# Kernel tuning notes

Measured on AMD Instinct MI355X. Metric: run time of the kernel, lower is better.

The kernel has to match this reference:

```python
import jax, jax.numpy as jnp
import numpy as np

B, T, E, H = 4, 2048, 1024, 16
S = E // H  # 64


def setup_inputs() -> dict:
    key = jax.random.key(0)
    ks = jax.random.split(key, 6)
    return {
        "x": jax.random.normal(ks[0], (B, T, E), dtype=jnp.float32),
        "Wk": jax.random.normal(ks[1], (S, S), dtype=jnp.float32) * (1.0 / np.sqrt(S)),
        "Wq": jax.random.normal(ks[2], (S, S), dtype=jnp.float32) * (1.0 / np.sqrt(S)),
        "Wv": jax.random.normal(ks[3], (S, S), dtype=jnp.float32) * (1.0 / np.sqrt(S)),
        "Wp": jax.random.normal(ks[4], (E, E), dtype=jnp.float32) * (1.0 / np.sqrt(E)),
        "bp": jnp.zeros((E,), dtype=jnp.float32),
    }


def reference(x, Wk, Wq, Wv, Wp, bp):
    b, t, e = x.shape
    h, s = H, S
    xh = x.reshape(b, t, h, s)
    # per-head projections share one (s,s) weight across all heads (torch Linear: y = x @ W.T)
    keys = jnp.einsum('bthi,oi->bhto', xh, Wk)     # (b,h,t,s)
    queries = jnp.einsum('bthi,oi->bhto', xh, Wq)
    values = jnp.einsum('bthi,oi->bhto', xh, Wv)
    scale = e ** 0.25  # q and k each divided by e^(1/4) -> net 1/sqrt(e)
    queries = queries / scale
    keys = keys / scale
    dot = jnp.einsum('bhqs,bhks->bhqk', queries, keys)  # (b,h,t,t)
    attn = jax.nn.softmax(dot, axis=-1)
    out = jnp.einsum('bhqk,bhks->bqhs', attn, values)   # (b,t,h,s)
    out = out.reshape(b, t, h * s)
    return jnp.einsum('bte,oe->bto', out, Wp) + bp
```

## Files before the change

kernel.cpp:

```cpp
#include <hip/hip_runtime.h>

#define Bv 4
#define Tv 2048
#define Ev 1024
#define Hv 16
#define Sv 64

typedef __attribute__((ext_vector_type(8))) short bf16x8;
typedef __attribute__((ext_vector_type(4))) float f32x4;

__device__ __forceinline__ ushort f2bf(float f) {
    unsigned u = __float_as_uint(f);
    u = (u + 0x7FFFu + ((u >> 16) & 1u)) >> 16;
    return (ushort)u;
}
__device__ __forceinline__ unsigned pk2(float a, float b) {
    return (unsigned)f2bf(a) | ((unsigned)f2bf(b) << 16);
}
__device__ __forceinline__ unsigned pk2r(float a, float b) {
    return ((__float_as_uint(a) + 0x8000u) >> 16)
         | ((__float_as_uint(b) + 0x8000u) & 0xffff0000u);
}

__device__ __forceinline__ void async16(void* lds, const void* g) {
    __builtin_amdgcn_global_load_lds(
        (const __attribute__((address_space(1))) unsigned int*)g,
        (__attribute__((address_space(3))) unsigned int*)lds, 16, 0, 0);
}

__global__ __launch_bounds__(256) void cast_kernel(
    const float* __restrict__ Wp, const float* __restrict__ Wq,
    const float* __restrict__ Wk, const float* __restrict__ Wv,
    ushort* __restrict__ Wpb, ushort* __restrict__ Wqb,
    ushort* __restrict__ Wkb, ushort* __restrict__ Wvb)
{
    int blk = blockIdx.x;
    if (blk < 1024) {
        int i = (blk * 256 + threadIdx.x) * 4;
        float4 v = *(const float4*)(Wp + i);
        ushort4 o;
        o.x = f2bf(v.x); o.y = f2bf(v.y); o.z = f2bf(v.z); o.w = f2bf(v.w);
        *(ushort4*)(Wpb + i) = o;
    } else {
        int p = blk - 1024;
        const float* src = (p == 0) ? Wq : ((p == 1) ? Wk : Wv);
        ushort* dst      = (p == 0) ? Wqb : ((p == 1) ? Wkb : Wvb);
        const float scale = (p == 0) ? 0.03125f * 1.4426950408889634f : 1.0f;
        #pragma unroll
        for (int it = 0; it < 4; ++it) {
            int i = (it * 256 + threadIdx.x) * 4;
            float4 v = *(const float4*)(src + i);
            ushort4 o;
            o.x = f2bf(v.x * scale); o.y = f2bf(v.y * scale);
            o.z = f2bf(v.z * scale); o.w = f2bf(v.w * scale);
            *(ushort4*)(dst + i) = o;
        }
    }
}

__global__ __launch_bounds__(192) void qkv_kernel(
    const float* __restrict__ x,
    const ushort* __restrict__ Wqb, const ushort* __restrict__ Wkb,
    const ushort* __restrict__ Wvb,
    ushort* __restrict__ Q, ushort* __restrict__ K, ushort* __restrict__ Vt)
{
    const int tid  = threadIdx.x;
    const int wave = tid >> 6;
    const int lane = tid & 63;
    const int m    = lane & 15;
    const int quad = lane >> 4;

    const ushort* Wsel = (wave == 0) ? Wqb : ((wave == 1) ? Wkb : Wvb);
    bf16x8 wf[4][2];
    #pragma unroll
    for (int ot = 0; ot < 4; ++ot)
        #pragma unroll
        for (int ks = 0; ks < 2; ++ks)
            wf[ot][ks] = *(const bf16x8*)&Wsel[(ot * 16 + m) * 64 + ks * 32 + quad * 8];

    const int tt = blockIdx.x >> 2;
    const int hg = blockIdx.x & 3;
    const int g0 = tt * 16;
    const int gm = g0 + m;
    const int b  = g0 >> 11;
    const int t0 = g0 & 2047;

    #pragma unroll
    for (int hi = 0; hi < 4; ++hi) {
        const int h  = hg * 4 + hi;
        const int bh = b * Hv + h;

        bf16x8 xf[2];
        #pragma unroll
        for (int ks = 0; ks < 2; ++ks) {
            const float* src = x + (size_t)gm * Ev + h * Sv + ks * 32 + quad * 8;
            float4 v0 = *(const float4*)src;
            float4 v1 = *(const float4*)(src + 4);
            unsigned pk[4];
            pk[0] = pk2(v0.x, v0.y); pk[1] = pk2(v0.z, v0.w);
            pk[2] = pk2(v1.x, v1.y); pk[3] = pk2(v1.z, v1.w);
            xf[ks] = *(bf16x8*)pk;
        }

        f32x4 acc[4];
        #pragma unroll
        for (int ot = 0; ot < 4; ++ot) acc[ot] = (f32x4){0.f, 0.f, 0.f, 0.f};

        if (wave < 2) {
            #pragma unroll
            for (int ks = 0; ks < 2; ++ks)
                #pragma unroll
                for (int ot = 0; ot < 4; ++ot)
                    acc[ot] = __builtin_amdgcn_mfma_f32_16x16x32_bf16(
                        wf[ot][ks], xf[ks], acc[ot], 0, 0, 0);
            ushort* dst = ((wave == 0) ? Q : K)
                        + ((size_t)bh * Tv + t0 + m) * Sv + quad * 4;
            #pragma unroll
            for (int ot = 0; ot < 4; ++ot) {
                uint2 w;
                w.x = pk2(acc[ot][0], acc[ot][1]);
                w.y = pk2(acc[ot][2], acc[ot][3]);
                *(uint2*)(dst + ot * 16) = w;
            }
        } else {
            #pragma unroll
            for (int ks = 0; ks < 2; ++ks)
                #pragma unroll
                for (int st = 0; st < 4; ++st)
                    acc[st] = __builtin_amdgcn_mfma_f32_16x16x32_bf16(
                        xf[ks], wf[st][ks], acc[st], 0, 0, 0);
            ushort* vr = Vt + ((size_t)bh * Sv + m) * Tv + t0 + quad * 4;
            #pragma unroll
            for (int st = 0; st < 4; ++st) {
                uint2 w;
                w.x = pk2(acc[st][0], acc[st][1]);
                w.y = pk2(acc[st][2], acc[st][3]);
                *(uint2*)(vr + (size_t)st * 16 * Tv) = w;
            }
        }
    }
}

__global__ __launch_bounds__(256, 4) void attn_kernel(
    const ushort* __restrict__ Q, const ushort* __restrict__ K,
    const ushort* __restrict__ Vt, ushort* __restrict__ O)
{
    __shared__ ushort kl[64 * 64];
    __shared__ ushort vl[64 * 64];
    __shared__ ushort pl[4][32 * 64];

    const int tid  = threadIdx.x;
    const int wave = tid >> 6;
    const int lane = tid & 63;
    const int m    = lane & 15;
    const int quad = lane >> 4;
    const int bh   = blockIdx.x & 63;
    const int q0   = (blockIdx.x >> 6) << 7;

    const ushort* Qb = Q + ((size_t)bh * Tv + q0 + wave * 32) * Sv;
    bf16x8 qf[2][2];
    #pragma unroll
    for (int g = 0; g < 2; ++g)
        #pragma unroll
        for (int ks = 0; ks < 2; ++ks)
            qf[g][ks] = *(const bf16x8*)&Qb[(g * 16 + m) * Sv + ks * 32 + quad * 8];

    f32x4 oa[2][4];
    float lsum[2] = {0.f, 0.f};
    #pragma unroll
    for (int g = 0; g < 2; ++g)
        #pragma unroll
        for (int nt = 0; nt < 4; ++nt)
            oa[g][nt] = (f32x4){0.f, 0.f, 0.f, 0.f};

    const ushort* Kb = K  + (size_t)bh * Tv * Sv;
    const ushort* Vb = Vt + (size_t)bh * Sv * Tv;
    ushort* pw = pl[wave];

    const int r0 = tid >> 3,         cg0 = (tid & 7) ^ (r0 & 7);
    const int r1 = (256 + tid) >> 3, cg1 = ((256 + tid) & 7) ^ (r1 & 7);
    const size_t koff0 = (size_t)r0 * Sv + cg0 * 8;
    const size_t koff1 = (size_t)r1 * Sv + cg1 * 8;
    const size_t voff0 = (size_t)r0 * Tv + cg0 * 8;
    const size_t voff1 = (size_t)r1 * Tv + cg1 * 8;
    const int mx = m & 7;

    for (int k0 = 0; k0 < Tv; k0 += 64) {
        __syncthreads();
        async16(&kl[(size_t)tid * 8],         Kb + (size_t)k0 * Sv + koff0);
        async16(&kl[((size_t)tid + 256) * 8], Kb + (size_t)k0 * Sv + koff1);
        async16(&vl[(size_t)tid * 8],         Vb + k0 + voff0);
        async16(&vl[((size_t)tid + 256) * 8], Vb + k0 + voff1);
        __syncthreads();

        #pragma unroll
        for (int nt = 0; nt < 4; ++nt) {
            const int krow = nt * 16 + m;
            bf16x8 a0 = *(const bf16x8*)&kl[krow * 64 + ((quad       ^ mx) * 8)];
            bf16x8 a1 = *(const bf16x8*)&kl[krow * 64 + (((4 + quad) ^ mx) * 8)];
            #pragma unroll
            for (int g = 0; g < 2; ++g) {
                f32x4 s = (f32x4){0.f, 0.f, 0.f, 0.f};
                s = __builtin_amdgcn_mfma_f32_16x16x32_bf16(a0, qf[g][0], s, 0, 0, 0);
                s = __builtin_amdgcn_mfma_f32_16x16x32_bf16(a1, qf[g][1], s, 0, 0, 0);
                float p0 = __builtin_amdgcn_exp2f(s[0]);
                float p1 = __builtin_amdgcn_exp2f(s[1]);
                float p2 = __builtin_amdgcn_exp2f(s[2]);
                float p3 = __builtin_amdgcn_exp2f(s[3]);
                lsum[g] += (p0 + p1) + (p2 + p3);
                uint2 w;
                w.x = pk2r(p0, p1);
                w.y = pk2r(p2, p3);
                *(uint2*)&pw[(g * 16 + m) * 64
                             + (((nt * 2 + (quad >> 1)) ^ mx) * 8)
                             + (quad & 1) * 4] = w;
            }
        }

        bf16x8 af[2][2];
        #pragma unroll
        for (int g = 0; g < 2; ++g) {
            af[g][0] = *(const bf16x8*)&pw[(g * 16 + m) * 64 + ((quad       ^ mx) * 8)];
            af[g][1] = *(const bf16x8*)&pw[(g * 16 + m) * 64 + (((4 + quad) ^ mx) * 8)];
        }
        #pragma unroll
        for (int nt = 0; nt < 4; ++nt) {
            const int vrow = nt * 16 + m;
            bf16x8 v0 = *(const bf16x8*)&vl[vrow * 64 + ((quad       ^ mx) * 8)];
            bf16x8 v1 = *(const bf16x8*)&vl[vrow * 64 + (((4 + quad) ^ mx) * 8)];
            #pragma unroll
            for (int g = 0; g < 2; ++g) {
                oa[g][nt] = __builtin_amdgcn_mfma_f32_16x16x32_bf16(af[g][0], v0, oa[g][nt], 0, 0, 0);
                oa[g][nt] = __builtin_amdgcn_mfma_f32_16x16x32_bf16(af[g][1], v1, oa[g][nt], 0, 0, 0);
            }
        }
    }

    #pragma unroll
    for (int g = 0; g < 2; ++g) {
        lsum[g] += __shfl_xor(lsum[g], 16, 64);
        lsum[g] += __shfl_xor(lsum[g], 32, 64);
    }
    float* ll = (float*)pw;
    if (lane < 16) {
        ll[lane]      = 1.0f / lsum[0];
        ll[16 + lane] = 1.0f / lsum[1];
    }

    const int b = bh >> 4, h = bh & 15;
    #pragma unroll
    for (int g = 0; g < 2; ++g)
        #pragma unroll
        for (int nt = 0; nt < 4; ++nt)
            #pragma unroll
            for (int r = 0; r < 4; ++r)
                O[((size_t)(b * Tv + q0 + wave * 32 + g * 16 + quad * 4 + r)) * Ev
                  + h * Sv + nt * 16 + m]
                    = f2bf(oa[g][nt][r] * ll[g * 16 + quad * 4 + r]);
}

__global__ __launch_bounds__(256) void proj_kernel(
    const ushort* __restrict__ A, const ushort* __restrict__ B,
    const float* __restrict__ bp, float* __restrict__ C)
{
    __shared__ ushort Asm[128 * 32];
    __shared__ ushort Bsm[128 * 32];
    const int tid  = threadIdx.x;
    const int wave = tid >> 6;
    const int lane = tid & 63;
    const int m    = lane & 15;
    const int quad = lane >> 4;
    const int wm   = wave >> 1;
    const int wn   = wave & 1;
    const int m0   = blockIdx.x * 128;
    const int n0   = blockIdx.y * 128;

    f32x4 acc[4][4];
    #pragma unroll
    for (int i = 0; i < 4; ++i)
        #pragma unroll
        for (int j = 0; j < 4; ++j)
            acc[i][j] = (f32x4){0.f, 0.f, 0.f, 0.f};

    for (int k0 = 0; k0 < Ev; k0 += 32) {
        __syncthreads();
        #pragma unroll
        for (int j = 0; j < 2; ++j) {
            int c   = j * 256 + tid;
            int row = c >> 2;
            int col = (c & 3) * 8;
            async16(&Asm[c * 8], &A[(size_t)(m0 + row) * Ev + k0 + col]);
            async16(&Bsm[c * 8], &B[(size_t)(n0 + row) * Ev + k0 + col]);
        }
        __syncthreads();

        bf16x8 af[4], bf[4];
        #pragma unroll
        for (int i = 0; i < 4; ++i)
            af[i] = *(const bf16x8*)&Asm[(wm * 64 + i * 16 + m) * 32 + quad * 8];
        #pragma unroll
        for (int j = 0; j < 4; ++j)
            bf[j] = *(const bf16x8*)&Bsm[(wn * 64 + j * 16 + m) * 32 + quad * 8];
        #pragma unroll
        for (int i = 0; i < 4; ++i)
            #pragma unroll
            for (int j = 0; j < 4; ++j)
                acc[i][j] = __builtin_amdgcn_mfma_f32_16x16x32_bf16(
                    af[i], bf[j], acc[i][j], 0, 0, 0);
    }

    float bbv[4];
    #pragma unroll
    for (int j = 0; j < 4; ++j)
        bbv[j] = bp[n0 + wn * 64 + j * 16 + m];

    #pragma unroll
    for (int i = 0; i < 4; ++i)
        #pragma unroll
        for (int j = 0; j < 4; ++j)
            #pragma unroll
            for (int r = 0; r < 4; ++r)
                C[(size_t)(m0 + wm * 64 + i * 16 + quad * 4 + r) * Ev
                  + n0 + wn * 64 + j * 16 + m] = acc[i][j][r] + bbv[j];
}

extern "C" void kernel_launch(void* const* d_in, const int* in_sizes, int n_in,
                              void* d_out, int out_size, void* d_ws, size_t ws_size,
                              hipStream_t stream) {
    const float* x  = (const float*)d_in[0];
    const float* Wk = (const float*)d_in[1];
    const float* Wq = (const float*)d_in[2];
    const float* Wv = (const float*)d_in[3];
    const float* Wp = (const float*)d_in[4];
    const float* bp = (const float*)d_in[5];
    float* out = (float*)d_out;

    ushort* Q   = (ushort*)d_ws;
    ushort* K   = Q   + 8388608;
    ushort* Vt  = K   + 8388608;
    ushort* O   = Vt  + 8388608;
    ushort* Wpb = O   + 8388608;
    ushort* Wqb = Wpb + 1048576;
    ushort* Wkb = Wqb + 4096;
    ushort* Wvb = Wkb + 4096;

    cast_kernel<<<1027, 256, 0, stream>>>(Wp, Wq, Wk, Wv, Wpb, Wqb, Wkb, Wvb);
    qkv_kernel<<<2048, 192, 0, stream>>>(x, Wqb, Wkb, Wvb, Q, K, Vt);
    attn_kernel<<<1024, 256, 0, stream>>>(Q, K, Vt, O);
    proj_kernel<<<dim3(64, 8), 256, 0, stream>>>(O, Wpb, bp, out);
}
```

Baseline: 229.6 us.

## Keep softmax probabilities in registers and feed PV with 16x16x16 MFMA

The attention kernel no longer writes exponentiated scores to a per-wave LDS buffer and reads them back as MFMA operands. The S-accumulator layout is reused directly as the A operand of 16x16x16 bf16 MFMAs, with V fragments read from LDS in a matching layout. The bf16 packing helpers are replaced by a truncating perm for P and the library round-to-nearest conversion elsewhere. The change removes an LDS round trip and frees LDS, but uses twice as many smaller MFMA instructions and truncates P instead of rounding it.

```diff
diff --git a/kernel.cpp b/kernel.cpp
--- a/kernel.cpp
+++ b/kernel.cpp
@@ -1,4 +1,5 @@
 #include <hip/hip_runtime.h>
+#include <hip/hip_bf16.h>
 
 #define Bv 4
 #define Tv 2048
@@ -7,19 +8,33 @@
 #define Sv 64
 
 typedef __attribute__((ext_vector_type(8))) short bf16x8;
+typedef __attribute__((ext_vector_type(4))) short bf16x4;
 typedef __attribute__((ext_vector_type(4))) float f32x4;
+
+#if __has_builtin(__builtin_amdgcn_mfma_f32_16x16x16_bf16)
+#define MFMA161616(a, b, c) __builtin_amdgcn_mfma_f32_16x16x16_bf16(a, b, c, 0, 0, 0)
+#elif __has_builtin(__builtin_amdgcn_mfma_f32_16x16x16bf16_1k)
+#define MFMA161616(a, b, c) __builtin_amdgcn_mfma_f32_16x16x16bf16_1k(a, b, c, 0, 0, 0)
+#else
+__device__ __forceinline__ f32x4 mfma161616_asm(bf16x4 a, bf16x4 b, f32x4 c) {
+    f32x4 d;
+    asm("v_mfma_f32_16x16x16_bf16 %0, %1, %2, %3" : "=v"(d) : "v"(a), "v"(b), "v"(c));
+    return d;
+}
+#define MFMA161616(a, b, c) mfma161616_asm(a, b, c)
+#endif
 
 __device__ __forceinline__ ushort f2bf(float f) {
     unsigned u = __float_as_uint(f);
     u = (u + 0x7FFFu + ((u >> 16) & 1u)) >> 16;
     return (ushort)u;
 }
-__device__ __forceinline__ unsigned pk2(float a, float b) {
-    return (unsigned)f2bf(a) | ((unsigned)f2bf(b) << 16);
-}
-__device__ __forceinline__ unsigned pk2r(float a, float b) {
-    return ((__float_as_uint(a) + 0x8000u) >> 16)
-         | ((__float_as_uint(b) + 0x8000u) & 0xffff0000u);
+__device__ __forceinline__ unsigned pkrn(float a, float b) {
+    __hip_bfloat162 t = __float22bfloat162_rn(make_float2(a, b));
+    unsigned r; __builtin_memcpy(&r, &t, 4); return r;
+}
+__device__ __forceinline__ unsigned pktr(float a, float b) {
+    return __builtin_amdgcn_perm(__float_as_uint(b), __float_as_uint(a), 0x07060302u);
 }
 
 __device__ __forceinline__ void async16(void* lds, const void* g) {
@@ -38,9 +53,8 @@
     if (blk < 1024) {
         int i = (blk * 256 + threadIdx.x) * 4;
         float4 v = *(const float4*)(Wp + i);
-        ushort4 o;
-        o.x = f2bf(v.x); o.y = f2bf(v.y); o.z = f2bf(v.z); o.w = f2bf(v.w);
-        *(ushort4*)(Wpb + i) = o;
+        uint2 o = {pkrn(v.x, v.y), pkrn(v.z, v.w)};
+        *(uint2*)(Wpb + i) = o;
     } else {
         int p = blk - 1024;
         const float* src = (p == 0) ? Wq : ((p == 1) ? Wk : Wv);
@@ -50,10 +64,8 @@
         for (int it = 0; it < 4; ++it) {
             int i = (it * 256 + threadIdx.x) * 4;
             float4 v = *(const float4*)(src + i);
-            ushort4 o;
-            o.x = f2bf(v.x * scale); o.y = f2bf(v.y * scale);
-            o.z = f2bf(v.z * scale); o.w = f2bf(v.w * scale);
-            *(ushort4*)(dst + i) = o;
+            uint2 o = {pkrn(v.x * scale, v.y * scale), pkrn(v.z * scale, v.w * scale)};
+            *(uint2*)(dst + i) = o;
         }
     }
 }
@@ -97,8 +109,8 @@
             float4 v0 = *(const float4*)src;
             float4 v1 = *(const float4*)(src + 4);
             unsigned pk[4];
-            pk[0] = pk2(v0.x, v0.y); pk[1] = pk2(v0.z, v0.w);
-            pk[2] = pk2(v1.x, v1.y); pk[3] = pk2(v1.z, v1.w);
+            pk[0] = pkrn(v0.x, v0.y); pk[1] = pkrn(v0.z, v0.w);
+            pk[2] = pkrn(v1.x, v1.y); pk[3] = pkrn(v1.z, v1.w);
             xf[ks] = *(bf16x8*)pk;
         }
 
@@ -117,9 +129,7 @@
                         + ((size_t)bh * Tv + t0 + m) * Sv + quad * 4;
             #pragma unroll
             for (int ot = 0; ot < 4; ++ot) {
-                uint2 w;
-                w.x = pk2(acc[ot][0], acc[ot][1]);
-                w.y = pk2(acc[ot][2], acc[ot][3]);
+                uint2 w = {pkrn(acc[ot][0], acc[ot][1]), pkrn(acc[ot][2], acc[ot][3])};
                 *(uint2*)(dst + ot * 16) = w;
             }
         } else {
@@ -132,9 +142,7 @@
             ushort* vr = Vt + ((size_t)bh * Sv + m) * Tv + t0 + quad * 4;
             #pragma unroll
             for (int st = 0; st < 4; ++st) {
-                uint2 w;
-                w.x = pk2(acc[st][0], acc[st][1]);
-                w.y = pk2(acc[st][2], acc[st][3]);
+                uint2 w = {pkrn(acc[st][0], acc[st][1]), pkrn(acc[st][2], acc[st][3])};
                 *(uint2*)(vr + (size_t)st * 16 * Tv) = w;
             }
         }
@@ -147,7 +155,7 @@
 {
     __shared__ ushort kl[64 * 64];
     __shared__ ushort vl[64 * 64];
-    __shared__ ushort pl[4][32 * 64];
+    __shared__ float  ll[4][32];
 
     const int tid  = threadIdx.x;
     const int wave = tid >> 6;
@@ -170,12 +178,11 @@
     #pragma unroll
     for (int g = 0; g < 2; ++g)
         #pragma unroll
-        for (int nt = 0; nt < 4; ++nt)
-            oa[g][nt] = (f32x4){0.f, 0.f, 0.f, 0.f};
+        for (int st = 0; st < 4; ++st)
+            oa[g][st] = (f32x4){0.f, 0.f, 0.f, 0.f};
 
     const ushort* Kb = K  + (size_t)bh * Tv * Sv;
     const ushort* Vb = Vt + (size_t)bh * Sv * Tv;
-    ushort* pw = pl[wave];
 
     const int r0 = tid >> 3,         cg0 = (tid & 7) ^ (r0 & 7);
     const int r1 = (256 + tid) >> 3, cg1 = ((256 + tid) & 7) ^ (r1 & 7);
@@ -193,6 +200,7 @@
         async16(&vl[((size_t)tid + 256) * 8], Vb + k0 + voff1);
         __syncthreads();
 
+        bf16x4 w[4][2];
         #pragma unroll
         for (int nt = 0; nt < 4; ++nt) {
             const int krow = nt * 16 + m;
@@ -208,31 +216,24 @@
                 float p2 = __builtin_amdgcn_exp2f(s[2]);
                 float p3 = __builtin_amdgcn_exp2f(s[3]);
                 lsum[g] += (p0 + p1) + (p2 + p3);
-                uint2 w;
-                w.x = pk2r(p0, p1);
-                w.y = pk2r(p2, p3);
-                *(uint2*)&pw[(g * 16 + m) * 64
-                             + (((nt * 2 + (quad >> 1)) ^ mx) * 8)
-                             + (quad & 1) * 4] = w;
+                unsigned pk[2] = {pktr(p0, p1), pktr(p2, p3)};
+                w[nt][g] = *(bf16x4*)pk;
             }
         }
 
-        bf16x8 af[2][2];
-        #pragma unroll
-        for (int g = 0; g < 2; ++g) {
-            af[g][0] = *(const bf16x8*)&pw[(g * 16 + m) * 64 + ((quad       ^ mx) * 8)];
-            af[g][1] = *(const bf16x8*)&pw[(g * 16 + m) * 64 + (((4 + quad) ^ mx) * 8)];
-        }
-        #pragma unroll
-        for (int nt = 0; nt < 4; ++nt) {
-            const int vrow = nt * 16 + m;
-            bf16x8 v0 = *(const bf16x8*)&vl[vrow * 64 + ((quad       ^ mx) * 8)];
-            bf16x8 v1 = *(const bf16x8*)&vl[vrow * 64 + (((4 + quad) ^ mx) * 8)];
-            #pragma unroll
-            for (int g = 0; g < 2; ++g) {
-                oa[g][nt] = __builtin_amdgcn_mfma_f32_16x16x32_bf16(af[g][0], v0, oa[g][nt], 0, 0, 0);
-                oa[g][nt] = __builtin_amdgcn_mfma_f32_16x16x32_bf16(af[g][1], v1, oa[g][nt], 0, 0, 0);
-            }
+        #pragma unroll
+        for (int st = 0; st < 4; ++st) {
+            const int srow = st * 16 + m;
+            bf16x4 vf[4];
+            #pragma unroll
+            for (int kt = 0; kt < 4; ++kt)
+                vf[kt] = *(const bf16x4*)&vl[srow * 64
+                           + (((2 * kt + (quad >> 1)) ^ mx) * 8) + (quad & 1) * 4];
+            #pragma unroll
+            for (int g = 0; g < 2; ++g)
+                #pragma unroll
+                for (int kt = 0; kt < 4; ++kt)
+                    oa[g][st] = MFMA161616(w[kt][g], vf[kt], oa[g][st]);
         }
     }
 
@@ -241,22 +242,21 @@
         lsum[g] += __shfl_xor(lsum[g], 16, 64);
         lsum[g] += __shfl_xor(lsum[g], 32, 64);
     }
-    float* ll = (float*)pw;
     if (lane < 16) {
-        ll[lane]      = 1.0f / lsum[0];
-        ll[16 + lane] = 1.0f / lsum[1];
+        ll[wave][lane]      = 1.0f / lsum[0];
+        ll[wave][16 + lane] = 1.0f / lsum[1];
     }
 
     const int b = bh >> 4, h = bh & 15;
     #pragma unroll
     for (int g = 0; g < 2; ++g)
         #pragma unroll
-        for (int nt = 0; nt < 4; ++nt)
+        for (int st = 0; st < 4; ++st)
             #pragma unroll
             for (int r = 0; r < 4; ++r)
                 O[((size_t)(b * Tv + q0 + wave * 32 + g * 16 + quad * 4 + r)) * Ev
-                  + h * Sv + nt * 16 + m]
-                    = f2bf(oa[g][nt][r] * ll[g * 16 + quad * 4 + r]);
+                  + h * Sv + st * 16 + m]
+                    = f2bf(oa[g][st][r] * ll[wave][g * 16 + quad * 4 + r]);
 }
 
 __global__ __launch_bounds__(256) void proj_kernel(
```

Measured after the change: 223.6 us. -2.6%, faster.
